# Kernel optimization log

Measured on AMD Instinct MI355X. Metric: run time of the kernel, lower is better.

Reference implementation:

```python
import jax, jax.numpy as jnp
import numpy as np

D_MODEL = 1024
NUM_HEADS = 16
HEAD_DIM = D_MODEL // NUM_HEADS  # 64
SEQ = 2048
BATCH = 4
LN_EPS = 1e-5


def setup_inputs() -> dict:
    key = jax.random.key(0)
    k_in, k_qkv, k_o, k_g = jax.random.split(key, 4)
    inputs = jax.random.normal(k_in, (BATCH, SEQ, D_MODEL), dtype=jnp.float32)
    mask = jnp.zeros((BATCH, 1, SEQ, SEQ), dtype=jnp.float32)  # additive mask
    # Realistic rotary embeddings (RoPE), duplicated-halves layout
    inv_freq = 1.0 / (10000.0 ** (jnp.arange(0, HEAD_DIM, 2, dtype=jnp.float32) / HEAD_DIM))
    pos = jnp.arange(SEQ, dtype=jnp.float32)
    freqs = pos[:, None] * inv_freq[None, :]            # [S, Dh/2]
    emb = jnp.concatenate([freqs, freqs], axis=-1)       # [S, Dh]
    cos = jnp.cos(emb)
    sin = jnp.sin(emb)
    # Parameters
    sd = 1.0 / np.sqrt(D_MODEL)
    w_qkv = jax.random.normal(k_qkv, (D_MODEL, 3 * D_MODEL), dtype=jnp.float32) * sd
    w_o = jax.random.normal(k_o, (D_MODEL, D_MODEL), dtype=jnp.float32) * sd
    ln_gamma = jnp.ones((D_MODEL,), dtype=jnp.float32)
    return {"inputs": inputs, "mask": mask, "cos": cos, "sin": sin,
            "ln_gamma": ln_gamma, "w_qkv": w_qkv, "w_o": w_o}


def _rotate_half(x):
    x1, x2 = jnp.split(x, 2, axis=-1)
    return jnp.concatenate([-x2, x1], axis=-1)


def reference(inputs, mask, cos, sin, ln_gamma, w_qkv, w_o):
    B, S, D = inputs.shape
    # Pre-attention LayerNorm (layer_id != 0), center=False -> no beta
    mu = jnp.mean(inputs, axis=-1, keepdims=True)
    var = jnp.mean(jnp.square(inputs - mu), axis=-1, keepdims=True)
    x = (inputs - mu) / jnp.sqrt(var + LN_EPS) * ln_gamma
    # Fused QKV projection, split into heads: [B, H, S, Dh]
    qkv = (x @ w_qkv).reshape(B, S, 3, NUM_HEADS, HEAD_DIM)
    qkv = jnp.transpose(qkv, (2, 0, 3, 1, 4))
    q, k, v = qkv[0], qkv[1], qkv[2]
    # RoPE
    c = cos.reshape(1, 1, S, HEAD_DIM)
    s = sin.reshape(1, 1, S, HEAD_DIM)
    q = q * c + _rotate_half(q) * s
    k = k * c + _rotate_half(k) * s
    # Scaled dot-product attention with additive mask
    scale = 1.0 / jnp.sqrt(jnp.asarray(HEAD_DIM, dtype=q.dtype))
    logits = jnp.einsum("bhqd,bhkd->bhqk", q, k) * scale + mask
    attn = jax.nn.softmax(logits, axis=-1)
    out = jnp.einsum("bhqk,bhkd->bhqd", attn, v)
    out = jnp.transpose(out, (0, 2, 1, 3)).reshape(B, S, D)
    return out @ w_o
```

## Files before the change

kernel.cpp:

```cpp
#include <hip/hip_runtime.h>
#include <stdint.h>

#define DEV __device__ __forceinline__

typedef __bf16 bf16x8 __attribute__((ext_vector_type(8)));
typedef float f32x4 __attribute__((ext_vector_type(4)));
typedef float f32x16 __attribute__((ext_vector_type(16)));

DEV unsigned short f2bf(float f) {
  union { float f; uint32_t u; } c; c.f = f;
  uint32_t u = c.u;
  u += 0x7FFFu + ((u >> 16) & 1u);
  return (unsigned short)(u >> 16);
}
DEV float bf2f(unsigned short h) {
  union { uint32_t u; float f; } c; c.u = ((uint32_t)h) << 16;
  return c.f;
}
DEV float u2f(uint32_t u) {
  union { uint32_t u; float f; } c; c.u = u;
  return c.f;
}
DEV bf16x8 ld8(const unsigned short* p) {
  uint4 u = *reinterpret_cast<const uint4*>(p);
  return __builtin_bit_cast(bf16x8, u);
}
DEV uint32_t cvtpk(float lo, float hi) {
  uint32_t r;
  asm("v_cvt_pk_bf16_f32 %0, %1, %2" : "=v"(r) : "v"(lo), "v"(hi));
  return r;
}
DEV void permswap(uint32_t& a, uint32_t& b) {
  asm("v_permlane32_swap_b32 %0, %1" : "+v"(a), "+v"(b));
}
DEV float exp2b(float x) { return __builtin_amdgcn_exp2f(x); }
DEV void gload16(const void* g, void* l) {
  __builtin_amdgcn_global_load_lds((const __attribute__((address_space(1))) void*)g,
                                   (__attribute__((address_space(3))) void*)l, 16, 0, 0);
}

template<int K, int N>
__global__ __launch_bounds__(256)
void transpose_cast_kernel(const float* __restrict__ in, unsigned short* __restrict__ out) {
  __shared__ float tile[64][65];
  const int bk = blockIdx.x % (K / 64);
  const int bn = blockIdx.x / (K / 64);
  const int k0 = bk * 64, n0 = bn * 64;
  const int t = threadIdx.x;
#pragma unroll
  for (int i = 0; i < 16; ++i) {
    int idx = t + i * 256;
    int kl = idx >> 6, nl = idx & 63;
    tile[kl][nl] = in[(size_t)(k0 + kl) * N + n0 + nl];
  }
  __syncthreads();
#pragma unroll
  for (int i = 0; i < 16; ++i) {
    int idx = t + i * 256;
    int nl = idx >> 6, kl = idx & 63;
    out[(size_t)(n0 + nl) * K + k0 + kl] = f2bf(tile[kl][nl]);
  }
}

__global__ __launch_bounds__(256)
void ln_kernel(const float* __restrict__ x, const float* __restrict__ gamma,
               unsigned short* __restrict__ y) {
  const int row = blockIdx.x;
  const int t = threadIdx.x;
  const float4 v = reinterpret_cast<const float4*>(x + (size_t)row * 1024)[t];
  float s  = v.x + v.y + v.z + v.w;
  float s2 = v.x * v.x + v.y * v.y + v.z * v.z + v.w * v.w;
#pragma unroll
  for (int off = 1; off < 64; off <<= 1) {
    s  += __shfl_xor(s, off);
    s2 += __shfl_xor(s2, off);
  }
  __shared__ float red[8];
  const int w = t >> 6, lane = t & 63;
  if (lane == 0) { red[w] = s; red[4 + w] = s2; }
  __syncthreads();
  s  = red[0] + red[1] + red[2] + red[3];
  s2 = red[4] + red[5] + red[6] + red[7];
  const float mu = s * (1.0f / 1024.0f);
  const float var = s2 * (1.0f / 1024.0f) - mu * mu;
  const float rstd = rsqrtf(var + 1e-5f);
  const float4 g = reinterpret_cast<const float4*>(gamma)[t];
  ushort4 o;
  o.x = f2bf((v.x - mu) * rstd * g.x);
  o.y = f2bf((v.y - mu) * rstd * g.y);
  o.z = f2bf((v.z - mu) * rstd * g.z);
  o.w = f2bf((v.w - mu) * rstd * g.w);
  reinterpret_cast<ushort4*>(y + (size_t)row * 1024)[t] = o;
}

template<int N_DIM>
__global__ __launch_bounds__(256)
void gemm_bt_kernel(const unsigned short* __restrict__ A,
                    const unsigned short* __restrict__ Bt,
                    float* __restrict__ Cout) {
  constexpr int K = 1024;
  __shared__ unsigned short a_lds[128 * 32];
  __shared__ unsigned short b_lds[128 * 32];
  const int t = threadIdx.x;
  const int w = t >> 6, l = t & 63;
  const int lrow = l & 15, lch = l >> 4;
  const int nbn = N_DIM / 128;
  const int m0 = (blockIdx.x / nbn) * 128;
  const int n0 = (blockIdx.x % nbn) * 128;
  const int wm = (w >> 1) * 64, wn = (w & 1) * 64;

  const int srow = t >> 2;
  const int schk = t & 3;
  const int scol = ((schk ^ (srow & 3)) << 3);
  const unsigned short* aS0 = A  + (size_t)(m0 + srow) * K + scol;
  const unsigned short* aS1 = A  + (size_t)(m0 + 64 + srow) * K + scol;
  const unsigned short* bS0 = Bt + (size_t)(n0 + srow) * K + scol;
  const unsigned short* bS1 = Bt + (size_t)(n0 + 64 + srow) * K + scol;
  unsigned short* aD0 = a_lds + (w * 16) * 32;
  unsigned short* aD1 = a_lds + (64 + w * 16) * 32;
  unsigned short* bD0 = b_lds + (w * 16) * 32;
  unsigned short* bD1 = b_lds + (64 + w * 16) * 32;

  f32x4 acc[4][4] = {};

  for (int k0 = 0; k0 < K; k0 += 32) {
    gload16(aS0 + k0, aD0);
    gload16(aS1 + k0, aD1);
    gload16(bS0 + k0, bD0);
    gload16(bS1 + k0, bD1);
    __syncthreads();
    bf16x8 af[4], bfr[4];
#pragma unroll
    for (int m = 0; m < 4; ++m) {
      int row = wm + m * 16 + lrow;
      af[m] = ld8(a_lds + row * 32 + ((lch ^ (lrow & 3)) << 3));
    }
#pragma unroll
    for (int n = 0; n < 4; ++n) {
      int row = wn + n * 16 + lrow;
      bfr[n] = ld8(b_lds + row * 32 + ((lch ^ (lrow & 3)) << 3));
    }
#pragma unroll
    for (int m = 0; m < 4; ++m)
#pragma unroll
      for (int n = 0; n < 4; ++n)
        acc[m][n] = __builtin_amdgcn_mfma_f32_16x16x32_bf16(af[m], bfr[n], acc[m][n], 0, 0, 0);
    __syncthreads();
  }

#pragma unroll
  for (int m = 0; m < 4; ++m) {
    const int grow0 = m0 + wm + m * 16 + lch * 4;
#pragma unroll
    for (int n = 0; n < 4; ++n) {
      const int gcol = n0 + wn + n * 16 + lrow;
#pragma unroll
      for (int r = 0; r < 4; ++r)
        Cout[(size_t)(grow0 + r) * N_DIM + gcol] = acc[m][n][r];
    }
  }
}

__global__ __launch_bounds__(256)
void gemm_qkv_rope_kernel(const unsigned short* __restrict__ A,
                          const unsigned short* __restrict__ Bt,
                          const float* __restrict__ cosb,
                          const float* __restrict__ sinb,
                          unsigned short* __restrict__ Qo,
                          unsigned short* __restrict__ Ko,
                          unsigned short* __restrict__ Vo) {
  constexpr int K = 1024;
  constexpr int N_DIM = 3072;
  __shared__ unsigned short a_lds[128 * 32];
  __shared__ unsigned short b_lds[128 * 32];
  const int t = threadIdx.x;
  const int w = t >> 6, l = t & 63;
  const int lrow = l & 15, lch = l >> 4;
  const int nbn = N_DIM / 128;
  const int m0 = (blockIdx.x / nbn) * 128;
  const int n0 = (blockIdx.x % nbn) * 128;
  const int wm = (w >> 1) * 64, wn = (w & 1) * 64;

  const int srow = t >> 2;
  const int schk = t & 3;
  const int scol = ((schk ^ (srow & 3)) << 3);
  const unsigned short* aS0 = A  + (size_t)(m0 + srow) * K + scol;
  const unsigned short* aS1 = A  + (size_t)(m0 + 64 + srow) * K + scol;
  const unsigned short* bS0 = Bt + (size_t)(n0 + srow) * K + scol;
  const unsigned short* bS1 = Bt + (size_t)(n0 + 64 + srow) * K + scol;
  unsigned short* aD0 = a_lds + (w * 16) * 32;
  unsigned short* aD1 = a_lds + (64 + w * 16) * 32;
  unsigned short* bD0 = b_lds + (w * 16) * 32;
  unsigned short* bD1 = b_lds + (64 + w * 16) * 32;

  f32x4 acc[4][4] = {};

  for (int k0 = 0; k0 < K; k0 += 32) {
    gload16(aS0 + k0, aD0);
    gload16(aS1 + k0, aD1);
    gload16(bS0 + k0, bD0);
    gload16(bS1 + k0, bD1);
    __syncthreads();
    bf16x8 af[4], bfr[4];
#pragma unroll
    for (int m = 0; m < 4; ++m) {
      int row = wm + m * 16 + lrow;
      af[m] = ld8(a_lds + row * 32 + ((lch ^ (lrow & 3)) << 3));
    }
#pragma unroll
    for (int n = 0; n < 4; ++n) {
      int row = wn + n * 16 + lrow;
      bfr[n] = ld8(b_lds + row * 32 + ((lch ^ (lrow & 3)) << 3));
    }
#pragma unroll
    for (int m = 0; m < 4; ++m)
#pragma unroll
      for (int n = 0; n < 4; ++n)
        acc[m][n] = __builtin_amdgcn_mfma_f32_16x16x32_bf16(af[m], bfr[n], acc[m][n], 0, 0, 0);
    __syncthreads();
  }

  const int b = m0 >> 11;
  const int sbase = (m0 & 2047) + wm;
  const int region = n0 >> 10;
  const int h = ((n0 & 1023) >> 6) + (w & 1);

  if (region < 2) {
    const float qs = (region == 0) ? 0.180336880f : 1.0f;
    unsigned short* dst = (region == 0 ? Qo : Ko) + (size_t)(b * 16 + h) * 2048 * 64;
#pragma unroll
    for (int m = 0; m < 4; ++m) {
#pragma unroll
      for (int r = 0; r < 4; ++r) {
        const int sg = sbase + m * 16 + lch * 4 + r;
        const float* crow = cosb + (size_t)sg * 64;
        const float* srow2 = sinb + (size_t)sg * 64;
        unsigned short* drow = dst + (size_t)sg * 64;
#pragma unroll
        for (int np = 0; np < 2; ++np) {
          const int d0 = np * 16 + lrow;
          const int d1 = d0 + 32;
          const float v0 = acc[m][np][r];
          const float v1 = acc[m][np + 2][r];
          const float r0 = v0 * crow[d0] - v1 * srow2[d0];
          const float r1 = v1 * crow[d1] + v0 * srow2[d1];
          drow[d0] = f2bf(r0 * qs);
          drow[d1] = f2bf(r1 * qs);
        }
      }
    }
  } else {
    unsigned short* dst = Vo + (size_t)(b * 16 + h) * 64 * 2048;
#pragma unroll
    for (int m = 0; m < 4; ++m) {
      const int sg0 = sbase + m * 16 + lch * 4;
#pragma unroll
      for (int np = 0; np < 4; ++np) {
        const int d = np * 16 + lrow;
        alignas(8) unsigned short o4[4];
#pragma unroll
        for (int r = 0; r < 4; ++r) o4[r] = f2bf(acc[m][np][r]);
        *(ushort4*)(dst + (size_t)d * 2048 + sg0) = *(ushort4*)o4;
      }
    }
  }
}

__global__ __launch_bounds__(256)
void mask_flags_kernel(const float* __restrict__ mask, unsigned char* __restrict__ flg) {
  const int bid = blockIdx.x;
  const int kvt = bid & 31, qc = (bid >> 5) & 31, b = bid >> 10;
  const int t = threadIdx.x;
  uint32_t orbits = 0;
  const int r = t >> 2, c0 = (t & 3) * 16;
  const float* src = mask + (size_t)b * (2048ull * 2048) + (size_t)(qc * 64 + r) * 2048 + kvt * 64 + c0;
#pragma unroll
  for (int i = 0; i < 4; ++i) {
    const float4 v = *(const float4*)(src + i * 4);
    orbits |= __float_as_uint(v.x) | __float_as_uint(v.y) |
              __float_as_uint(v.z) | __float_as_uint(v.w);
  }
  const int nz = __syncthreads_or(orbits != 0u);
  if (t == 0) flg[(size_t)(b * 32 + kvt) * 32 + qc] = (unsigned char)(nz != 0);
}

__global__ __launch_bounds__(256)
void mask_retile_kernel(const float* __restrict__ mask, unsigned short* __restrict__ mrs,
                        const unsigned char* __restrict__ flg) {
  const int bid = blockIdx.x;
  const int kvt = bid & 31, qc = (bid >> 5) & 31, b = bid >> 10;
  if (!flg[(size_t)(b * 32 + kvt) * 32 + qc]) return;
  const int t = threadIdx.x;
  __shared__ float tile[64][72];
  {
    const int r = t >> 2, c0 = (t & 3) * 16;
    const float* src = mask + (size_t)b * (2048ull * 2048) + (size_t)(qc * 64 + r) * 2048 + kvt * 64 + c0;
#pragma unroll
    for (int i = 0; i < 4; ++i) {
      const float4 v = *(const float4*)(src + i * 4);
      *(float4*)&tile[r][c0 + i * 4] = v;
    }
  }
  __syncthreads();
  const int cid = t >> 5;
  const int n = cid >> 2, jj = (cid >> 1) & 1, hi = cid & 1;
  const int qq0 = (t & 31) * 2;
  const int cb = n * 32 + jj * 16 + hi * 4;
  unsigned short* dst = mrs + (((size_t)(b * 32 + kvt) * 8 + cid) * 2048 + qc * 64) * 8;
#pragma unroll
  for (int qo = 0; qo < 2; ++qo) {
    const int q = qq0 + qo;
    alignas(16) unsigned short o8[8];
#pragma unroll
    for (int v = 0; v < 8; ++v) {
      const int col = cb + (v >> 2) * 8 + (v & 3);
      o8[v] = f2bf(tile[q][col] * 1.44269504f);
    }
    *(uint4*)(dst + (size_t)q * 8) = *(uint4*)o8;
  }
}

__global__ __launch_bounds__(256)
void attn_kernel(const unsigned short* __restrict__ Q,
                 const unsigned short* __restrict__ Kg,
                 const unsigned short* __restrict__ Vt,
                 const unsigned short* __restrict__ mrs,
                 const unsigned char* __restrict__ flg,
                 unsigned short* __restrict__ O) {
  const int t = threadIdx.x, w = t >> 6, l = t & 63;
  const int lq = l & 31, hi = l >> 5;
  const int bid = blockIdx.x;
  const int x = bid & 7, y = bid >> 3;
  const int bh = x * 8 + (y & 7), qb = y >> 3;
  const int b = bh >> 4, h = bh & 15;
  const int q0 = qb * 128 + w * 32;

  const unsigned short* Qb = Q  + (size_t)bh * (2048 * 64);
  const unsigned short* Kb = Kg + (size_t)bh * (2048 * 64);
  const unsigned short* Vb = Vt + (size_t)bh * (64 * 2048);
  const unsigned short* ml = mrs + (size_t)b * 4194304 + (size_t)hi * 16384 + (size_t)(q0 + lq) * 8;
  const unsigned char* fb = flg + (size_t)(b * 32) * 32 + qb * 2;

  __shared__ unsigned short k_lds[2][64 * 64];
  __shared__ unsigned short v_lds[2][64 * 64];

  bf16x8 qf[4];
  {
    const unsigned short* qp = Qb + (size_t)(q0 + lq) * 64 + hi * 8;
#pragma unroll
    for (int c = 0; c < 4; ++c) qf[c] = ld8(qp + c * 16);
  }
  bf16x8 ones;
  {
    const uint4 ou = { 0x3F803F80u, 0x3F803F80u, 0x3F803F80u, 0x3F803F80u };
    ones = __builtin_bit_cast(bf16x8, ou);
  }

  const int srow = t >> 2, sl0 = (t & 3) * 2, sl1 = sl0 + 1;
  const unsigned short* ks = Kb + (size_t)srow * 64 + sl0 * 8;
  const unsigned short* vs = Vb + (size_t)srow * 2048 + sl0 * 8;
  const int wd0 = srow * 64 + ((sl0 ^ (srow & 7)) << 3);
  const int wd1 = srow * 64 + ((sl1 ^ (srow & 7)) << 3);

  uint4 ka0 = *(const uint4*)ks;
  uint4 ka1 = *(const uint4*)(ks + 8);
  uint4 va0 = *(const uint4*)vs;
  uint4 va1 = *(const uint4*)(vs + 8);
  *(uint4*)(k_lds[0] + wd0) = ka0;
  *(uint4*)(k_lds[0] + wd1) = ka1;
  *(uint4*)(v_lds[0] + wd0) = va0;
  *(uint4*)(v_lds[0] + wd1) = va1;

  f32x16 ot0 = {}, ot1 = {};
  f32x16 st_sum = {};
  int cur = 0;
  const int lsw = lq & 7;

  uint4 mA[4], mB[4];

  auto do_tile = [&](int kv0, uint4 (&mcur)[4], uint4 (&mnext)[4],
                     bool hm, bool hmn) {
    __syncthreads();
    const bool more = (kv0 + 64) < 2048;
    if (more) {
      ka0 = *(const uint4*)(ks + (size_t)(kv0 + 64) * 64);
      ka1 = *(const uint4*)(ks + (size_t)(kv0 + 64) * 64 + 8);
      va0 = *(const uint4*)(vs + kv0 + 64);
      va1 = *(const uint4*)(vs + kv0 + 64 + 8);
      if (hmn) {
        const unsigned short* mp = ml + (size_t)(kv0 + 64) * 2048;
#pragma unroll
        for (int c2 = 0; c2 < 4; ++c2) mnext[c2] = *(const uint4*)(mp + c2 * 32768);
      }
    }

    f32x16 st0 = {}, st1 = {};
    if (hm) {
#pragma unroll
      for (int jj = 0; jj < 2; ++jj) {
        const uint4 u0 = mcur[jj];
        const uint4 u1 = mcur[2 + jj];
#pragma unroll
        for (int wv = 0; wv < 4; ++wv) {
          const uint32_t w0 = ((const uint32_t*)&u0)[wv];
          const uint32_t w1 = ((const uint32_t*)&u1)[wv];
          st0[jj * 8 + wv * 2]     = u2f(w0 << 16);
          st0[jj * 8 + wv * 2 + 1] = u2f(w0 & 0xffff0000u);
          st1[jj * 8 + wv * 2]     = u2f(w1 << 16);
          st1[jj * 8 + wv * 2 + 1] = u2f(w1 & 0xffff0000u);
        }
      }
    }

    const unsigned short* kb = k_lds[cur];
    __builtin_amdgcn_s_setprio(1);
#pragma unroll
    for (int c = 0; c < 4; ++c) {
      const int so = (((2 * c + hi) ^ lsw) << 3);
      const bf16x8 kf0 = ld8(kb + lq * 64 + so);
      const bf16x8 kf1 = ld8(kb + (32 + lq) * 64 + so);
      st0 = __builtin_amdgcn_mfma_f32_32x32x16_bf16(kf0, qf[c], st0, 0, 0, 0);
      st1 = __builtin_amdgcn_mfma_f32_32x32x16_bf16(kf1, qf[c], st1, 0, 0, 0);
    }
    __builtin_amdgcn_s_setprio(0);

#pragma unroll
    for (int r = 0; r < 16; ++r) {
      st0[r] = exp2b(st0[r]);
      st1[r] = exp2b(st1[r]);
    }

    bf16x8 pa[4];
#pragma unroll
    for (int c = 0; c < 4; ++c) {
      const int e8 = (c & 1) * 8;
      uint32_t A01, B01, A23, B23;
      if (c < 2) {
        A01 = cvtpk(st0[e8 + 0], st0[e8 + 1]);
        B01 = cvtpk(st0[e8 + 4], st0[e8 + 5]);
        A23 = cvtpk(st0[e8 + 2], st0[e8 + 3]);
        B23 = cvtpk(st0[e8 + 6], st0[e8 + 7]);
      } else {
        A01 = cvtpk(st1[e8 + 0], st1[e8 + 1]);
        B01 = cvtpk(st1[e8 + 4], st1[e8 + 5]);
        A23 = cvtpk(st1[e8 + 2], st1[e8 + 3]);
        B23 = cvtpk(st1[e8 + 6], st1[e8 + 7]);
      }
      permswap(A01, B01);
      permswap(A23, B23);
      const uint4 pw = { A01, A23, B01, B23 };
      pa[c] = __builtin_bit_cast(bf16x8, pw);
    }

    if (more) {
      unsigned short* kn = k_lds[cur ^ 1];
      unsigned short* vn = v_lds[cur ^ 1];
      *(uint4*)(kn + wd0) = ka0;
      *(uint4*)(kn + wd1) = ka1;
      *(uint4*)(vn + wd0) = va0;
      *(uint4*)(vn + wd1) = va1;
    }

    const unsigned short* vb = v_lds[cur];
    __builtin_amdgcn_s_setprio(1);
#pragma unroll
    for (int c = 0; c < 4; ++c) {
      const int so = (((2 * c + hi) ^ lsw) << 3);
      const bf16x8 vf0 = ld8(vb + lq * 64 + so);
      const bf16x8 vf1 = ld8(vb + (32 + lq) * 64 + so);
      ot0 = __builtin_amdgcn_mfma_f32_32x32x16_bf16(vf0, pa[c], ot0, 0, 0, 0);
      ot1 = __builtin_amdgcn_mfma_f32_32x32x16_bf16(vf1, pa[c], ot1, 0, 0, 0);
      st_sum = __builtin_amdgcn_mfma_f32_32x32x16_bf16(ones, pa[c], st_sum, 0, 0, 0);
    }
    __builtin_amdgcn_s_setprio(0);
    cur ^= 1;
  };

  unsigned int bm = 0;
  for (int kvt = 0; kvt < 32; ++kvt) bm |= fb[kvt * 32] | fb[kvt * 32 + 1];

  if (bm == 0) {
    for (int kv0 = 0; kv0 < 2048; kv0 += 128) {
      do_tile(kv0, mA, mB, false, false);
      do_tile(kv0 + 64, mB, mA, false, false);
    }
  } else {
    bool hmA = (fb[0] | fb[1]) != 0;
    if (hmA) {
#pragma unroll
      for (int c2 = 0; c2 < 4; ++c2) mA[c2] = *(const uint4*)(ml + c2 * 32768);
    }
    bool hmB = false;
    for (int kv0 = 0; kv0 < 2048; kv0 += 128) {
      const int tB = (kv0 >> 6) + 1;
      hmB = (kv0 + 64 < 2048) && ((fb[tB * 32] | fb[tB * 32 + 1]) != 0);
      do_tile(kv0, mA, mB, hmA, hmB);
      const int tA = tB + 1;
      hmA = (kv0 + 128 < 2048) && ((fb[tA * 32] | fb[tA * 32 + 1]) != 0);
      do_tile(kv0 + 64, mB, mA, hmB, hmA);
    }
  }

  const float inv = 1.0f / st_sum[0];
  unsigned short* ob = O + ((size_t)(b * 2048 + q0 + lq) * 16 + h) * 64 + hi * 4;
#pragma unroll
  for (int td = 0; td < 2; ++td) {
#pragma unroll
    for (int rr = 0; rr < 4; ++rr) {
      ushort4 ov;
      if (td == 0) {
        ov.x = f2bf(ot0[rr * 4 + 0] * inv);
        ov.y = f2bf(ot0[rr * 4 + 1] * inv);
        ov.z = f2bf(ot0[rr * 4 + 2] * inv);
        ov.w = f2bf(ot0[rr * 4 + 3] * inv);
      } else {
        ov.x = f2bf(ot1[rr * 4 + 0] * inv);
        ov.y = f2bf(ot1[rr * 4 + 1] * inv);
        ov.z = f2bf(ot1[rr * 4 + 2] * inv);
        ov.w = f2bf(ot1[rr * 4 + 3] * inv);
      }
      *(ushort4*)(ob + td * 32 + rr * 8) = ov;
    }
  }
}

extern "C" void kernel_launch(void* const* d_in, const int* in_sizes, int n_in,
                              void* d_out, int out_size, void* d_ws, size_t ws_size,
                              hipStream_t stream) {
  (void)in_sizes; (void)n_in; (void)out_size; (void)ws_size;
  const float* x     = (const float*)d_in[0];
  const float* mask  = (const float*)d_in[1];
  const float* cosb  = (const float*)d_in[2];
  const float* sinb  = (const float*)d_in[3];
  const float* gamma = (const float*)d_in[4];
  const float* w_qkv = (const float*)d_in[5];
  const float* w_o   = (const float*)d_in[6];

  char* ws = (char*)d_ws;
  unsigned short* x_bf   = (unsigned short*)(ws);
  unsigned short* wqkvT  = (unsigned short*)(ws + 16777216);
  unsigned short* woT    = (unsigned short*)(ws + 23068672);
  unsigned short* mask_rs = (unsigned short*)(ws + 25165824);
  unsigned char*  flags   = (unsigned char*)(ws + 25165824 + 33554432);
  unsigned short* q_r    = (unsigned short*)(ws + 75497472);
  unsigned short* k_r    = (unsigned short*)(ws + 92274688);
  unsigned short* v_t    = (unsigned short*)(ws + 109051904);
  unsigned short* attn   = (unsigned short*)(ws + 125829120);

  transpose_cast_kernel<1024, 3072><<<dim3(16 * 48), dim3(256), 0, stream>>>(w_qkv, wqkvT);
  transpose_cast_kernel<1024, 1024><<<dim3(16 * 16), dim3(256), 0, stream>>>(w_o, woT);
  ln_kernel<<<dim3(8192), dim3(256), 0, stream>>>(x, gamma, x_bf);
  gemm_qkv_rope_kernel<<<dim3(64 * 24), dim3(256), 0, stream>>>(x_bf, wqkvT, cosb, sinb, q_r, k_r, v_t);
  mask_flags_kernel<<<dim3(4096), dim3(256), 0, stream>>>(mask, flags);
  mask_retile_kernel<<<dim3(4096), dim3(256), 0, stream>>>(mask, mask_rs, flags);
  attn_kernel<<<dim3(1024), dim3(256), 0, stream>>>(q_r, k_r, v_t, mask_rs, flags, attn);
  gemm_bt_kernel<1024><<<dim3(64 * 8), dim3(256), 0, stream>>>(attn, woT, (float*)d_out);
}
```

Before: 233.2 us.

## Remap GEMM blocks across XCDs, fuse mask prep kernels, double KV tile loads in attention

Both GEMM kernels now permute blockIdx so consecutive blocks spread across the 8 XCDs in contiguous chunks, aiming for better L2 reuse of A/B tiles. The separate mask flag and retile kernels are merged into one pass that reads the mask once and retiles only nonzero blocks. The attention kernel now stages 128 KV rows per barrier (two 64-row sub-tiles per LDS buffer), halving the number of syncthreads and issuing larger prefetches. In exchange it uses twice the LDS, which may reduce occupancy, and it loads mask values without prefetching them.

```diff
diff --git a/kernel.cpp b/kernel.cpp
--- a/kernel.cpp
+++ b/kernel.cpp
@@ -99,14 +99,15 @@
                     const unsigned short* __restrict__ Bt,
                     float* __restrict__ Cout) {
   constexpr int K = 1024;
+  constexpr int nbn = N_DIM / 128;
   __shared__ unsigned short a_lds[128 * 32];
   __shared__ unsigned short b_lds[128 * 32];
   const int t = threadIdx.x;
   const int w = t >> 6, l = t & 63;
   const int lrow = l & 15, lch = l >> 4;
-  const int nbn = N_DIM / 128;
-  const int m0 = (blockIdx.x / nbn) * 128;
-  const int n0 = (blockIdx.x % nbn) * 128;
+  const int rid = (blockIdx.x & 7) * (8 * nbn) + (blockIdx.x >> 3);
+  const int m0 = (rid / nbn) * 128;
+  const int n0 = (rid % nbn) * 128;
   const int wm = (w >> 1) * 64, wn = (w & 1) * 64;
 
   const int srow = t >> 2;
@@ -170,16 +171,17 @@
                           unsigned short* __restrict__ Ko,
                           unsigned short* __restrict__ Vo) {
   constexpr int K = 1024;
-  constexpr int N_DIM = 3072;
+  constexpr int nbn = 24;
   __shared__ unsigned short a_lds[128 * 32];
   __shared__ unsigned short b_lds[128 * 32];
   const int t = threadIdx.x;
   const int w = t >> 6, l = t & 63;
   const int lrow = l & 15, lch = l >> 4;
-  const int nbn = N_DIM / 128;
-  const int m0 = (blockIdx.x / nbn) * 128;
-  const int n0 = (blockIdx.x % nbn) * 128;
+  const int rid = (blockIdx.x & 7) * 192 + (blockIdx.x >> 3);
+  const int m0 = (rid / nbn) * 128;
+  const int n0 = (rid % nbn) * 128;
   const int wm = (w >> 1) * 64, wn = (w & 1) * 64;
+  (void)wn;
 
   const int srow = t >> 2;
   const int schk = t & 3;
@@ -209,7 +211,7 @@
     }
 #pragma unroll
     for (int n = 0; n < 4; ++n) {
-      int row = wn + n * 16 + lrow;
+      int row = (w & 1) * 64 + n * 16 + lrow;
       bfr[n] = ld8(b_lds + row * 32 + ((lch ^ (lrow & 3)) << 3));
     }
 #pragma unroll
@@ -267,40 +269,28 @@
 }
 
 __global__ __launch_bounds__(256)
-void mask_flags_kernel(const float* __restrict__ mask, unsigned char* __restrict__ flg) {
+void mask_prep_kernel(const float* __restrict__ mask, unsigned short* __restrict__ mrs,
+                      unsigned char* __restrict__ flg) {
   const int bid = blockIdx.x;
   const int kvt = bid & 31, qc = (bid >> 5) & 31, b = bid >> 10;
   const int t = threadIdx.x;
-  uint32_t orbits = 0;
   const int r = t >> 2, c0 = (t & 3) * 16;
   const float* src = mask + (size_t)b * (2048ull * 2048) + (size_t)(qc * 64 + r) * 2048 + kvt * 64 + c0;
+  float4 v4[4];
+  uint32_t orbits = 0;
 #pragma unroll
   for (int i = 0; i < 4; ++i) {
-    const float4 v = *(const float4*)(src + i * 4);
-    orbits |= __float_as_uint(v.x) | __float_as_uint(v.y) |
-              __float_as_uint(v.z) | __float_as_uint(v.w);
+    v4[i] = *(const float4*)(src + i * 4);
+    orbits |= __float_as_uint(v4[i].x) | __float_as_uint(v4[i].y) |
+              __float_as_uint(v4[i].z) | __float_as_uint(v4[i].w);
   }
   const int nz = __syncthreads_or(orbits != 0u);
   if (t == 0) flg[(size_t)(b * 32 + kvt) * 32 + qc] = (unsigned char)(nz != 0);
-}
-
-__global__ __launch_bounds__(256)
-void mask_retile_kernel(const float* __restrict__ mask, unsigned short* __restrict__ mrs,
-                        const unsigned char* __restrict__ flg) {
-  const int bid = blockIdx.x;
-  const int kvt = bid & 31, qc = (bid >> 5) & 31, b = bid >> 10;
-  if (!flg[(size_t)(b * 32 + kvt) * 32 + qc]) return;
-  const int t = threadIdx.x;
+  if (!nz) return;
+
   __shared__ float tile[64][72];
-  {
-    const int r = t >> 2, c0 = (t & 3) * 16;
-    const float* src = mask + (size_t)b * (2048ull * 2048) + (size_t)(qc * 64 + r) * 2048 + kvt * 64 + c0;
-#pragma unroll
-    for (int i = 0; i < 4; ++i) {
-      const float4 v = *(const float4*)(src + i * 4);
-      *(float4*)&tile[r][c0 + i * 4] = v;
-    }
-  }
+#pragma unroll
+  for (int i = 0; i < 4; ++i) *(float4*)&tile[r][c0 + i * 4] = v4[i];
   __syncthreads();
   const int cid = t >> 5;
   const int n = cid >> 2, jj = (cid >> 1) & 1, hi = cid & 1;
@@ -341,8 +331,8 @@
   const unsigned short* ml = mrs + (size_t)b * 4194304 + (size_t)hi * 16384 + (size_t)(q0 + lq) * 8;
   const unsigned char* fb = flg + (size_t)(b * 32) * 32 + qb * 2;
 
-  __shared__ unsigned short k_lds[2][64 * 64];
-  __shared__ unsigned short v_lds[2][64 * 64];
+  __shared__ unsigned short k_lds[2][2][64 * 64];
+  __shared__ unsigned short v_lds[2][2][64 * 64];
 
   bf16x8 qf[4];
   {
@@ -356,50 +346,60 @@
     ones = __builtin_bit_cast(bf16x8, ou);
   }
 
-  const int srow = t >> 2, sl0 = (t & 3) * 2, sl1 = sl0 + 1;
-  const unsigned short* ks = Kb + (size_t)srow * 64 + sl0 * 8;
-  const unsigned short* vs = Vb + (size_t)srow * 2048 + sl0 * 8;
+  const int srow = t >> 2;
+  const int sl0 = (t & 3) * 2, sl1 = sl0 + 1;
+  const int vsub = (t & 3) >> 1, vcb = ((t & 3) & 1) * 4;
+  const unsigned short* ks0 = Kb + (size_t)srow * 64 + sl0 * 8;
+  const unsigned short* ks1 = Kb + (size_t)(64 + srow) * 64 + sl0 * 8;
+  const unsigned short* vsrc = Vb + (size_t)srow * 2048 + (t & 3) * 32;
   const int wd0 = srow * 64 + ((sl0 ^ (srow & 7)) << 3);
   const int wd1 = srow * 64 + ((sl1 ^ (srow & 7)) << 3);
-
-  uint4 ka0 = *(const uint4*)ks;
-  uint4 ka1 = *(const uint4*)(ks + 8);
-  uint4 va0 = *(const uint4*)vs;
-  uint4 va1 = *(const uint4*)(vs + 8);
-  *(uint4*)(k_lds[0] + wd0) = ka0;
-  *(uint4*)(k_lds[0] + wd1) = ka1;
-  *(uint4*)(v_lds[0] + wd0) = va0;
-  *(uint4*)(v_lds[0] + wd1) = va1;
+  const int wv0 = srow * 64 + (((vcb + 0) ^ (srow & 7)) << 3);
+  const int wv1 = srow * 64 + (((vcb + 1) ^ (srow & 7)) << 3);
+  const int wv2 = srow * 64 + (((vcb + 2) ^ (srow & 7)) << 3);
+  const int wv3 = srow * 64 + (((vcb + 3) ^ (srow & 7)) << 3);
+
+  uint4 ka0 = *(const uint4*)ks0;
+  uint4 ka1 = *(const uint4*)(ks0 + 8);
+  uint4 ka2 = *(const uint4*)ks1;
+  uint4 ka3 = *(const uint4*)(ks1 + 8);
+  uint4 va0 = *(const uint4*)vsrc;
+  uint4 va1 = *(const uint4*)(vsrc + 8);
+  uint4 va2 = *(const uint4*)(vsrc + 16);
+  uint4 va3 = *(const uint4*)(vsrc + 24);
+  *(uint4*)(k_lds[0][0] + wd0) = ka0;
+  *(uint4*)(k_lds[0][0] + wd1) = ka1;
+  *(uint4*)(k_lds[0][1] + wd0) = ka2;
+  *(uint4*)(k_lds[0][1] + wd1) = ka3;
+  {
+    unsigned short* vd = v_lds[0][vsub];
+    *(uint4*)(vd + wv0) = va0;
+    *(uint4*)(vd + wv1) = va1;
+    *(uint4*)(vd + wv2) = va2;
+    *(uint4*)(vd + wv3) = va3;
+  }
 
   f32x16 ot0 = {}, ot1 = {};
   f32x16 st_sum = {};
   int cur = 0;
   const int lsw = lq & 7;
 
-  uint4 mA[4], mB[4];
-
-  auto do_tile = [&](int kv0, uint4 (&mcur)[4], uint4 (&mnext)[4],
-                     bool hm, bool hmn) {
-    __syncthreads();
-    const bool more = (kv0 + 64) < 2048;
-    if (more) {
-      ka0 = *(const uint4*)(ks + (size_t)(kv0 + 64) * 64);
-      ka1 = *(const uint4*)(ks + (size_t)(kv0 + 64) * 64 + 8);
-      va0 = *(const uint4*)(vs + kv0 + 64);
-      va1 = *(const uint4*)(vs + kv0 + 64 + 8);
-      if (hmn) {
-        const unsigned short* mp = ml + (size_t)(kv0 + 64) * 2048;
-#pragma unroll
-        for (int c2 = 0; c2 < 4; ++c2) mnext[c2] = *(const uint4*)(mp + c2 * 32768);
-      }
-    }
-
+  unsigned int bmap = 0;
+  for (int kvt = 0; kvt < 32; ++kvt)
+    if (fb[kvt * 32] | fb[kvt * 32 + 1]) bmap |= (1u << kvt);
+
+  auto do_sub = [&](const unsigned short* kb, const unsigned short* vb,
+                    int kvt64, bool hm) {
     f32x16 st0 = {}, st1 = {};
     if (hm) {
+      const unsigned short* mp = ml + (size_t)kvt64 * 131072;
+      uint4 mc[4];
+#pragma unroll
+      for (int c2 = 0; c2 < 4; ++c2) mc[c2] = *(const uint4*)(mp + c2 * 32768);
 #pragma unroll
       for (int jj = 0; jj < 2; ++jj) {
-        const uint4 u0 = mcur[jj];
-        const uint4 u1 = mcur[2 + jj];
+        const uint4 u0 = mc[jj];
+        const uint4 u1 = mc[2 + jj];
 #pragma unroll
         for (int wv = 0; wv < 4; ++wv) {
           const uint32_t w0 = ((const uint32_t*)&u0)[wv];
@@ -412,7 +412,6 @@
       }
     }
 
-    const unsigned short* kb = k_lds[cur];
     __builtin_amdgcn_s_setprio(1);
 #pragma unroll
     for (int c = 0; c < 4; ++c) {
@@ -452,16 +451,6 @@
       pa[c] = __builtin_bit_cast(bf16x8, pw);
     }
 
-    if (more) {
-      unsigned short* kn = k_lds[cur ^ 1];
-      unsigned short* vn = v_lds[cur ^ 1];
-      *(uint4*)(kn + wd0) = ka0;
-      *(uint4*)(kn + wd1) = ka1;
-      *(uint4*)(vn + wd0) = va0;
-      *(uint4*)(vn + wd1) = va1;
-    }
-
-    const unsigned short* vb = v_lds[cur];
     __builtin_amdgcn_s_setprio(1);
 #pragma unroll
     for (int c = 0; c < 4; ++c) {
@@ -473,32 +462,43 @@
       st_sum = __builtin_amdgcn_mfma_f32_32x32x16_bf16(ones, pa[c], st_sum, 0, 0, 0);
     }
     __builtin_amdgcn_s_setprio(0);
+  };
+
+  for (int kv0 = 0; kv0 < 2048; kv0 += 128) {
+    __syncthreads();
+    const bool more = (kv0 + 128) < 2048;
+    if (more) {
+      const size_t off = (size_t)(kv0 + 128) * 64;
+      ka0 = *(const uint4*)(ks0 + off);
+      ka1 = *(const uint4*)(ks0 + off + 8);
+      ka2 = *(const uint4*)(ks1 + off);
+      ka3 = *(const uint4*)(ks1 + off + 8);
+      const unsigned short* vp = vsrc + kv0 + 128;
+      va0 = *(const uint4*)vp;
+      va1 = *(const uint4*)(vp + 8);
+      va2 = *(const uint4*)(vp + 16);
+      va3 = *(const uint4*)(vp + 24);
+    }
+    const int kvt2 = kv0 >> 6;
+
+    do_sub(k_lds[cur][0], v_lds[cur][0], kvt2, (bmap >> kvt2) & 1u);
+
+    if (more) {
+      unsigned short* k0d = k_lds[cur ^ 1][0];
+      unsigned short* k1d = k_lds[cur ^ 1][1];
+      *(uint4*)(k0d + wd0) = ka0;
+      *(uint4*)(k0d + wd1) = ka1;
+      *(uint4*)(k1d + wd0) = ka2;
+      *(uint4*)(k1d + wd1) = ka3;
+      unsigned short* vd = v_lds[cur ^ 1][vsub];
+      *(uint4*)(vd + wv0) = va0;
+      *(uint4*)(vd + wv1) = va1;
+      *(uint4*)(vd + wv2) = va2;
+      *(uint4*)(vd + wv3) = va3;
+    }
+
+    do_sub(k_lds[cur][1], v_lds[cur][1], kvt2 + 1, (bmap >> (kvt2 + 1)) & 1u);
     cur ^= 1;
-  };
-
-  unsigned int bm = 0;
-  for (int kvt = 0; kvt < 32; ++kvt) bm |= fb[kvt * 32] | fb[kvt * 32 + 1];
-
-  if (bm == 0) {
-    for (int kv0 = 0; kv0 < 2048; kv0 += 128) {
-      do_tile(kv0, mA, mB, false, false);
-      do_tile(kv0 + 64, mB, mA, false, false);
-    }
-  } else {
-    bool hmA = (fb[0] | fb[1]) != 0;
-    if (hmA) {
-#pragma unroll
-      for (int c2 = 0; c2 < 4; ++c2) mA[c2] = *(const uint4*)(ml + c2 * 32768);
-    }
-    bool hmB = false;
-    for (int kv0 = 0; kv0 < 2048; kv0 += 128) {
-      const int tB = (kv0 >> 6) + 1;
-      hmB = (kv0 + 64 < 2048) && ((fb[tB * 32] | fb[tB * 32 + 1]) != 0);
-      do_tile(kv0, mA, mB, hmA, hmB);
-      const int tA = tB + 1;
-      hmA = (kv0 + 128 < 2048) && ((fb[tA * 32] | fb[tA * 32 + 1]) != 0);
-      do_tile(kv0 + 64, mB, mA, hmB, hmA);
-    }
   }
 
   const float inv = 1.0f / st_sum[0];
@@ -551,8 +551,7 @@
   transpose_cast_kernel<1024, 1024><<<dim3(16 * 16), dim3(256), 0, stream>>>(w_o, woT);
   ln_kernel<<<dim3(8192), dim3(256), 0, stream>>>(x, gamma, x_bf);
   gemm_qkv_rope_kernel<<<dim3(64 * 24), dim3(256), 0, stream>>>(x_bf, wqkvT, cosb, sinb, q_r, k_r, v_t);
-  mask_flags_kernel<<<dim3(4096), dim3(256), 0, stream>>>(mask, flags);
-  mask_retile_kernel<<<dim3(4096), dim3(256), 0, stream>>>(mask, mask_rs, flags);
+  mask_prep_kernel<<<dim3(4096), dim3(256), 0, stream>>>(mask, mask_rs, flags);
   attn_kernel<<<dim3(1024), dim3(256), 0, stream>>>(q_r, k_r, v_t, mask_rs, flags, attn);
   gemm_bt_kernel<1024><<<dim3(64 * 8), dim3(256), 0, stream>>>(attn, woT, (float*)d_out);
 }
```

After: 245.2 us. +5.2%, slower.
